# Kernel tuning notes

Measured on AMD Instinct MI355X. Metric: run time of the kernel, lower is better.

## Reference

```python
import jax, jax.numpy as jnp
import numpy as np

B, T, C, H = 2, 2048, 1024, 16
D = C // H  # head_dim = 64


def setup_inputs() -> dict:
    key = jax.random.key(0)
    ks = jax.random.split(key, 5)
    x = jax.random.normal(ks[0], (B, T, C), dtype=jnp.float32)
    # fused QKV projection: Linear(C, 3C)
    W_qkv = jax.random.normal(ks[1], (C, 3 * C), dtype=jnp.float32) / np.sqrt(C)
    b_qkv = jax.random.normal(ks[2], (3 * C,), dtype=jnp.float32) * 0.02
    # output projection: Linear(C, C)
    W_proj = jax.random.normal(ks[3], (C, C), dtype=jnp.float32) / np.sqrt(C)
    b_proj = jax.random.normal(ks[4], (C,), dtype=jnp.float32) * 0.02
    return {"x": x, "W_qkv": W_qkv, "b_qkv": b_qkv, "W_proj": W_proj, "b_proj": b_proj}


def reference(x, W_qkv, b_qkv, W_proj, b_proj):
    # fused QKV projection
    qkv = jnp.einsum("btc,cd->btd", x, W_qkv) + b_qkv  # [B,T,3C]
    q, k, v = jnp.split(qkv, 3, axis=-1)
    # [B,T,C] -> [B,H,T,D]
    def to_heads(t):
        return t.reshape(B, T, H, D).transpose(0, 2, 1, 3)
    q, k, v = to_heads(q), to_heads(k), to_heads(v)
    # causal scaled dot-product attention (SDPA default scale = 1/sqrt(head_dim))
    scale = 1.0 / np.sqrt(D).astype(np.float32)
    scores = jnp.einsum("bhqd,bhkd->bhqk", q, k) * scale  # [B,H,T,T]
    causal = jnp.tril(jnp.ones((T, T), dtype=bool))
    scores = jnp.where(causal, scores, jnp.finfo(scores.dtype).min)
    attn = jax.nn.softmax(scores, axis=-1)
    out = jnp.einsum("bhqk,bhkd->bhqd", attn, v)  # [B,H,T,D]
    out = out.transpose(0, 2, 1, 3).reshape(B, T, C)
    # output projection
    return jnp.einsum("btc,cd->btd", out, W_proj) + b_proj
```

## Files before the change

kernel.cpp:

```cpp
#include <hip/hip_runtime.h>
#include <hip/hip_bf16.h>

typedef __attribute__((ext_vector_type(8))) __bf16 bf16x8;
typedef __attribute__((ext_vector_type(8))) short short8;
typedef __attribute__((ext_vector_type(4))) float f32x4;
typedef __attribute__((ext_vector_type(16))) float f32x16;
typedef __attribute__((ext_vector_type(4))) short sh4;

typedef __attribute__((address_space(1))) void GVoid;
typedef __attribute__((address_space(3))) void LVoid;

#define NEGBIG (-1e30f)
#define SCL 0.18033688011112042f

constexpr int TT = 2048, CC = 1024, HH = 16, DD = 64, C3 = 3072;

__device__ __forceinline__ unsigned short f2bf(float f) {
  unsigned int i = __float_as_uint(f);
  return (unsigned short)((i + 0x7FFFu + ((i >> 16) & 1u)) >> 16);
}
__device__ __forceinline__ void async16(const void* g, void* l) {
  __builtin_amdgcn_global_load_lds((GVoid*)g, (LVoid*)l, 16, 0, 0);
}

__global__ __launch_bounds__(256) void cvt_bf16(
    const float* __restrict__ in, unsigned short* __restrict__ out, int n8)
{
  const int i = blockIdx.x * 256 + threadIdx.x;
  if (i >= n8) return;
  const float* p = in + (size_t)i * 8;
  f32x4 a = *(const f32x4*)p, b = *(const f32x4*)(p + 4);
  sh4 r0, r1;
  ((unsigned short*)&r0)[0] = f2bf(a[0]); ((unsigned short*)&r0)[1] = f2bf(a[1]);
  ((unsigned short*)&r0)[2] = f2bf(a[2]); ((unsigned short*)&r0)[3] = f2bf(a[3]);
  ((unsigned short*)&r1)[0] = f2bf(b[0]); ((unsigned short*)&r1)[1] = f2bf(b[1]);
  ((unsigned short*)&r1)[2] = f2bf(b[2]); ((unsigned short*)&r1)[3] = f2bf(b[3]);
  *(sh4*)(out + (size_t)i * 8) = r0;
  *(sh4*)(out + (size_t)i * 8 + 4) = r1;
}

__global__ __launch_bounds__(256) void transpose_cvt(
    const float* __restrict__ in, unsigned short* __restrict__ out, int R, int Cd)
{
  __shared__ __align__(16) unsigned short tile[64 * 72];
  const int r0 = blockIdx.y * 64, c0 = blockIdx.x * 64;
  const int tid = threadIdx.x;
#pragma unroll
  for (int r = 0; r < 2; ++r) {
    const int elem = r * 2048 + tid * 8;
    const int ii = elem >> 6, jj = elem & 63;
    const float* p = in + (size_t)(r0 + ii) * Cd + c0 + jj;
    f32x4 a = *(const f32x4*)p, b = *(const f32x4*)(p + 4);
    short8 v;
    ((unsigned short*)&v)[0] = f2bf(a[0]); ((unsigned short*)&v)[1] = f2bf(a[1]);
    ((unsigned short*)&v)[2] = f2bf(a[2]); ((unsigned short*)&v)[3] = f2bf(a[3]);
    ((unsigned short*)&v)[4] = f2bf(b[0]); ((unsigned short*)&v)[5] = f2bf(b[1]);
    ((unsigned short*)&v)[6] = f2bf(b[2]); ((unsigned short*)&v)[7] = f2bf(b[3]);
    *(short8*)&tile[ii * 72 + jj] = v;
  }
  __syncthreads();
#pragma unroll
  for (int r = 0; r < 2; ++r) {
    const int elem = r * 2048 + tid * 8;
    const int jj = elem >> 6, ii0 = elem & 63;
    short8 v;
#pragma unroll
    for (int e = 0; e < 8; ++e) ((unsigned short*)&v)[e] = tile[(ii0 + e) * 72 + jj];
    *(short8*)&out[(size_t)(c0 + jj) * R + r0 + ii0] = v;
  }
}

template <int MODE>
__global__ __launch_bounds__(256) void gemm_bt(
    const unsigned short* __restrict__ A,
    const unsigned short* __restrict__ Bt,
    const float* __restrict__ bias,
    void* __restrict__ Cp, unsigned short* __restrict__ Vt,
    int M, int N, int K, int lda)
{
  __shared__ __align__(16) unsigned short sA[2][128 * 32];
  __shared__ __align__(16) unsigned short sB[2][128 * 32];
  const int tid = threadIdx.x;
  const int w = tid >> 6, l = tid & 63, ln = l & 15, quad = l >> 4;
  const int wm = w >> 1, wn = w & 1;
  const int m0 = blockIdx.y * 128, n0 = blockIdx.x * 128;
  f32x4 acc[4][4] = {};

  const int elem0 = tid * 8;
  const int ar0 = elem0 >> 5, ac0 = elem0 & 31;
  const int ar1 = (2048 + elem0) >> 5, ac1 = ac0;

  async16(A  + (size_t)(m0 + ar0) * lda + ac0, &sA[0][w * 512]);
  async16(Bt + (size_t)(n0 + ar0) * K   + ac0, &sB[0][w * 512]);
  async16(A  + (size_t)(m0 + ar1) * lda + ac1, &sA[0][2048 + w * 512]);
  async16(Bt + (size_t)(n0 + ar1) * K   + ac1, &sB[0][2048 + w * 512]);
  __syncthreads();

  int buf = 0;
  for (int k0 = 0; k0 < K; k0 += 32, buf ^= 1) {
    if (k0 + 32 < K) {
      const int nb = buf ^ 1, kn = k0 + 32;
      async16(A  + (size_t)(m0 + ar0) * lda + kn + ac0, &sA[nb][w * 512]);
      async16(Bt + (size_t)(n0 + ar0) * K   + kn + ac0, &sB[nb][w * 512]);
      async16(A  + (size_t)(m0 + ar1) * lda + kn + ac1, &sA[nb][2048 + w * 512]);
      async16(Bt + (size_t)(n0 + ar1) * K   + kn + ac1, &sB[nb][2048 + w * 512]);
    }

    bf16x8 af[4], bfr[4];
#pragma unroll
    for (int i = 0; i < 4; i++)
      af[i] = *(const bf16x8*)&sA[buf][(wm * 64 + i * 16 + ln) * 32 + quad * 8];
#pragma unroll
    for (int j = 0; j < 4; j++)
      bfr[j] = *(const bf16x8*)&sB[buf][(wn * 64 + j * 16 + ln) * 32 + quad * 8];
#pragma unroll
    for (int i = 0; i < 4; i++)
#pragma unroll
      for (int j = 0; j < 4; j++)
        acc[i][j] = __builtin_amdgcn_mfma_f32_16x16x32_bf16(af[i], bfr[j], acc[i][j], 0, 0, 0);

    __syncthreads();
  }

  float bj[4];
#pragma unroll
  for (int j = 0; j < 4; j++) bj[j] = bias[n0 + wn * 64 + j * 16 + ln];

#pragma unroll
  for (int i = 0; i < 4; i++) {
#pragma unroll
    for (int j = 0; j < 4; j++) {
      const int gn = n0 + wn * 64 + j * 16 + ln;
      if (MODE == 0 && gn >= 2048) {
        const int hh = (gn >> 6) & 15, dd = gn & 63;
        const int gm0 = m0 + wm * 64 + i * 16 + quad * 4;
        const int bb = gm0 >> 11, t0 = gm0 & 2047;
        sh4 rv;
#pragma unroll
        for (int g = 0; g < 4; ++g)
          ((unsigned short*)&rv)[g] = f2bf(acc[i][j][g] + bj[j]);
        *(sh4*)&Vt[((size_t)((bb * HH + hh) * DD + dd)) * TT + t0] = rv;
      } else {
#pragma unroll
        for (int g = 0; g < 4; ++g) {
          const int gm = m0 + wm * 64 + i * 16 + quad * 4 + g;
          float v = acc[i][j][g] + bj[j];
          if (MODE == 0) {
            if (gn < 1024) v *= SCL;
            ((unsigned short*)Cp)[(size_t)gm * 2048 + gn] = f2bf(v);
          } else {
            ((float*)Cp)[(size_t)gm * N + gn] = v;
          }
        }
      }
    }
  }
}

__global__ __launch_bounds__(256) void gemm_n64(
    const unsigned short* __restrict__ A,
    const unsigned short* __restrict__ Bt,
    const float* __restrict__ bias,
    float* __restrict__ Cp, int M, int N, int K, int lda)
{
  __shared__ __align__(16) unsigned short sA[2][128 * 32];
  __shared__ __align__(16) unsigned short sB[2][64 * 32];
  const int tid = threadIdx.x;
  const int w = tid >> 6, l = tid & 63, ln = l & 15, quad = l >> 4;
  const int wm = w >> 1, wn = w & 1;
  const int m0 = blockIdx.y * 128, n0 = blockIdx.x * 64;
  f32x4 acc[4][2] = {};

  const int elem0 = tid * 8;
  const int ar0 = elem0 >> 5, ac0 = elem0 & 31;
  const int ar1 = (2048 + elem0) >> 5, ac1 = ac0;

  async16(A  + (size_t)(m0 + ar0) * lda + ac0, &sA[0][w * 512]);
  async16(A  + (size_t)(m0 + ar1) * lda + ac1, &sA[0][2048 + w * 512]);
  async16(Bt + (size_t)(n0 + ar0) * K   + ac0, &sB[0][w * 512]);
  __syncthreads();

  int buf = 0;
  for (int k0 = 0; k0 < K; k0 += 32, buf ^= 1) {
    if (k0 + 32 < K) {
      const int nb = buf ^ 1, kn = k0 + 32;
      async16(A  + (size_t)(m0 + ar0) * lda + kn + ac0, &sA[nb][w * 512]);
      async16(A  + (size_t)(m0 + ar1) * lda + kn + ac1, &sA[nb][2048 + w * 512]);
      async16(Bt + (size_t)(n0 + ar0) * K   + kn + ac0, &sB[nb][w * 512]);
    }

    bf16x8 af[4], bfr[2];
#pragma unroll
    for (int i = 0; i < 4; i++)
      af[i] = *(const bf16x8*)&sA[buf][(wm * 64 + i * 16 + ln) * 32 + quad * 8];
#pragma unroll
    for (int j = 0; j < 2; j++)
      bfr[j] = *(const bf16x8*)&sB[buf][(wn * 32 + j * 16 + ln) * 32 + quad * 8];
#pragma unroll
    for (int i = 0; i < 4; i++)
#pragma unroll
      for (int j = 0; j < 2; j++)
        acc[i][j] = __builtin_amdgcn_mfma_f32_16x16x32_bf16(af[i], bfr[j], acc[i][j], 0, 0, 0);

    __syncthreads();
  }

  float bj[2];
#pragma unroll
  for (int j = 0; j < 2; j++) bj[j] = bias[n0 + wn * 32 + j * 16 + ln];

#pragma unroll
  for (int i = 0; i < 4; i++)
#pragma unroll
    for (int g = 0; g < 4; ++g) {
      const int gm = m0 + wm * 64 + i * 16 + quad * 4 + g;
#pragma unroll
      for (int j = 0; j < 2; j++) {
        const int gn = n0 + wn * 32 + j * 16 + ln;
        Cp[(size_t)gm * N + gn] = acc[i][j][g] + bj[j];
      }
    }
}

__global__ __launch_bounds__(512) void attn2g(
    unsigned short* __restrict__ QK, const unsigned short* __restrict__ Vt)
{
  __shared__ __align__(16) unsigned short kt[2][2][64 * 72];
  __shared__ __align__(16) unsigned short vt[2][3][64 * 72];
  __shared__ float Ox[4][2][16][64];
  __shared__ float Lx[4][64];
  const int lid = blockIdx.y * gridDim.x + blockIdx.x;
  const int xcd = lid & 7, idx = lid >> 3;
  const int bh = xcd * 4 + (idx & 3);
  const int pair = idx >> 2;
  const int b = bh >> 4, h = bh & 15;
  const int tid = threadIdx.x;
  const int grp = tid >> 8, gtid = tid & 255;
  const int wg = (tid >> 6) & 3, l = tid & 63;
  const int c = l & 31, h2 = l >> 5;
  unsigned short*       Qp = QK + (size_t)b * TT * 2048 + h * DD;
  const unsigned short* Kp = QK + (size_t)b * TT * 2048 + CC + h * DD;
  const unsigned short* Vh = Vt + (size_t)bh * DD * TT;
  const int si0 = gtid >> 3, so = (gtid & 7) * 8;

  for (int ph = 0; ph < 2; ++ph) {
    const int qt = ph ? 15 - pair : pair;
    const int qbase = qt * 128 + wg * 32;
    const int qm = qbase + c - 4 * h2;
    bf16x8 qv[4];
#pragma unroll
    for (int ds = 0; ds < 4; ++ds)
      qv[ds] = *(const bf16x8*)&Qp[(size_t)(qbase + c) * 2048 + ds * 16 + h2 * 8];

    f32x16 oacc[2] = {};
    bf16x8 pA[4] = {};
    float lsum = 0.0f;
    const int nslot = qt + 1;
    int vm1 = 2, v0 = 0, vp1 = 1;

    __syncthreads();
#pragma unroll
    for (int r = 0; r < 2; ++r) {
      const int si = si0 + 32 * r;
      *(short8*)&kt[grp][0][si * 72 + so] =
          *(const short8*)&Kp[(size_t)(grp * 64 + si) * 2048 + so];
      *(short8*)&vt[grp][0][si * 72 + so] =
          *(const short8*)&Vh[(size_t)si * TT + grp * 64 + so];
    }
    __syncthreads();

    for (int slot = 0; slot < nslot; ++slot) {
      const int kb = 2 * slot + grp;
      const int ck = slot & 1;
      short8 pk[2], pv[2];
      if (slot + 1 < nslot) {
        const int kbn = kb + 2;
#pragma unroll
        for (int r = 0; r < 2; ++r) {
          const int si = si0 + 32 * r;
          pk[r] = *(const short8*)&Kp[(size_t)(kbn * 64 + si) * 2048 + so];
          pv[r] = *(const short8*)&Vh[(size_t)si * TT + kbn * 64 + so];
        }
      }
      const bool qk_act = (kb * 64 <= qbase + 31);
      f32x16 sacc[2];
      if (qk_act) {
        __builtin_amdgcn_s_setprio(1);
#pragma unroll
        for (int kg = 0; kg < 2; ++kg) {
          f32x16 sa = {};
#pragma unroll
          for (int ds = 0; ds < 4; ++ds) {
            bf16x8 kf = *(const bf16x8*)&kt[grp][ck][(kg * 32 + c) * 72 + ds * 16 + h2 * 8];
            sa = __builtin_amdgcn_mfma_f32_32x32x16_bf16(kf, qv[ds], sa, 0, 0, 0);
          }
          sacc[kg] = sa;
        }
        __builtin_amdgcn_s_setprio(0);
      }
      if (slot > 0 && (kb - 2) * 64 <= qbase + 31) {
        const unsigned short* vp = vt[grp][vm1];
        __builtin_amdgcn_s_setprio(1);
#pragma unroll
        for (int dg = 0; dg < 2; ++dg)
#pragma unroll
          for (int ks = 0; ks < 4; ++ks) {
            bf16x8 vf = *(const bf16x8*)&vp[(dg * 32 + c) * 72 + ks * 16 + h2 * 8];
            oacc[dg] = __builtin_amdgcn_mfma_f32_32x32x16_bf16(pA[ks], vf, oacc[dg], 0, 0, 0);
          }
        __builtin_amdgcn_s_setprio(0);
      }
      if (qk_act) {
        const bool need_mask = (kb * 64 + 63 > qbase);
        float pe[2][16];
#pragma unroll
        for (int kg = 0; kg < 2; ++kg)
#pragma unroll
          for (int rr = 0; rr < 16; ++rr) {
            float sv = sacc[kg][rr];
            if (need_mask) {
              const int krel = kb * 64 + kg * 32 + (rr & 3) + 8 * (rr >> 2);
              if (krel > qm) sv = NEGBIG;
            }
            float e;
            asm("v_exp_f32 %0, %1" : "=v"(e) : "v"(sv));
            pe[kg][rr] = e;
            lsum += e;
          }
        unsigned W0[2][4], W1[2][4];
#pragma unroll
        for (int kg = 0; kg < 2; ++kg)
#pragma unroll
          for (int r4 = 0; r4 < 4; ++r4) {
            asm("v_cvt_pk_bf16_f32 %0, %1, %2"
                : "=v"(W0[kg][r4]) : "v"(pe[kg][4 * r4 + 0]), "v"(pe[kg][4 * r4 + 1]));
            asm("v_cvt_pk_bf16_f32 %0, %1, %2"
                : "=v"(W1[kg][r4]) : "v"(pe[kg][4 * r4 + 2]), "v"(pe[kg][4 * r4 + 3]));
          }
#pragma unroll
        for (int ks = 0; ks < 4; ++ks) {
          const int kg = ks >> 1, sel = ks & 1;
          unsigned a0 = W0[kg][2 * sel], b0 = W0[kg][2 * sel + 1];
          unsigned a1 = W1[kg][2 * sel], b1 = W1[kg][2 * sel + 1];
          asm("v_permlane32_swap_b32 %0, %1" : "+v"(a0), "+v"(b0));
          asm("v_permlane32_swap_b32 %0, %1" : "+v"(a1), "+v"(b1));
          unsigned wds[4] = {a0, a1, b0, b1};
          pA[ks] = *(const bf16x8*)wds;
        }
      }
      if (slot + 1 < nslot) {
#pragma unroll
        for (int r = 0; r < 2; ++r) {
          const int si = si0 + 32 * r;
          *(short8*)&kt[grp][1 - ck][si * 72 + so] = pk[r];
          *(short8*)&vt[grp][vp1][si * 72 + so] = pv[r];
        }
      }
      __syncthreads();
      const int t_ = vm1; vm1 = v0; v0 = vp1; vp1 = t_;
    }
    const int kb_last = 2 * qt + grp;
    if (kb_last * 64 <= qbase + 31) {
      const unsigned short* vp = vt[grp][vm1];
#pragma unroll
      for (int dg = 0; dg < 2; ++dg)
#pragma unroll
        for (int ks = 0; ks < 4; ++ks) {
          bf16x8 vf = *(const bf16x8*)&vp[(dg * 32 + c) * 72 + ks * 16 + h2 * 8];
          oacc[dg] = __builtin_amdgcn_mfma_f32_32x32x16_bf16(pA[ks], vf, oacc[dg], 0, 0, 0);
        }
    }
    lsum += __shfl_xor(lsum, 32);
    if (grp == 1) {
#pragma unroll
      for (int dg = 0; dg < 2; ++dg)
#pragma unroll
        for (int rr = 0; rr < 16; ++rr) Ox[wg][dg][rr][l] = oacc[dg][rr];
      Lx[wg][l] = lsum;
    }
    __syncthreads();
    if (grp == 0) {
      const float inv = 1.0f / (lsum + Lx[wg][l]);
#pragma unroll
      for (int dg = 0; dg < 2; ++dg)
#pragma unroll
        for (int rr = 0; rr < 16; ++rr) oacc[dg][rr] += Ox[wg][dg][rr][l];
#pragma unroll
      for (int rr = 0; rr < 16; ++rr) {
        const int q_rel = (rr & 3) + 8 * (rr >> 2) + 4 * h2;
        const float iq = __shfl(inv, q_rel);
        const size_t trow = qbase + q_rel;
#pragma unroll
        for (int dg = 0; dg < 2; ++dg)
          Qp[trow * 2048 + dg * 32 + c] = f2bf(oacc[dg][rr] * iq);
      }
    }
  }
}

extern "C" void kernel_launch(void* const* d_in, const int* in_sizes, int n_in,
                              void* d_out, int out_size, void* d_ws, size_t ws_size,
                              hipStream_t stream)
{
  (void)in_sizes; (void)n_in; (void)out_size; (void)ws_size;
  const float* x     = (const float*)d_in[0];
  const float* Wqkv  = (const float*)d_in[1];
  const float* bqkv  = (const float*)d_in[2];
  const float* Wproj = (const float*)d_in[3];
  const float* bproj = (const float*)d_in[4];

  unsigned short* QK     = (unsigned short*)d_ws;
  unsigned short* WqkvT  = QK + (size_t)4096 * 2048;
  unsigned short* WprojT = WqkvT;
  unsigned short* Vt = (unsigned short*)d_out;
  unsigned short* xb = Vt + (size_t)32 * 64 * 2048;

  cvt_bf16<<<dim3(4096 * 1024 / 8 / 256), 256, 0, stream>>>(x, xb, 4096 * 1024 / 8);
  transpose_cvt<<<dim3(C3 / 64, CC / 64), 256, 0, stream>>>(Wqkv, WqkvT, CC, C3);
  gemm_bt<0><<<dim3(C3 / 128, 4096 / 128), 256, 0, stream>>>(
      xb, WqkvT, bqkv, QK, Vt, 4096, C3, CC, CC);
  transpose_cvt<<<dim3(CC / 64, CC / 64), 256, 0, stream>>>(Wproj, WprojT, CC, CC);
  attn2g<<<dim3(8, 2 * HH), 512, 0, stream>>>(QK, Vt);
  gemm_n64<<<dim3(CC / 64, 4096 / 128), 256, 0, stream>>>(
      QK, WprojT, bproj, (float*)d_out, 4096, CC, CC, 2048);
}
```

Before: 180.5 us.

## Process two KV tiles per barrier with a 4-deep LDS ring buffer

Restructures the attention inner loop so each iteration handles two key/value tiles between barriers, using a four-slot shared-memory ring for K and V per group, which halves the number of __syncthreads calls. The old software pipeline, which overlapped the PV MFMA of the previous tile with the QK of the current one, is replaced by a straight per-tile compute lambda that does QK, softmax and PV in sequence. The LDS arrays are merged into one union buffer that is reused for the final cross-group reduction, so total LDS grows (144 KB). Risks are lower occupancy and the loss of the cross-tile MFMA/VALU overlap.

```diff
diff --git a/kernel.cpp b/kernel.cpp
--- a/kernel.cpp
+++ b/kernel.cpp
@@ -225,10 +225,9 @@
 __global__ __launch_bounds__(512) void attn2g(
     unsigned short* __restrict__ QK, const unsigned short* __restrict__ Vt)
 {
-  __shared__ __align__(16) unsigned short kt[2][2][64 * 72];
-  __shared__ __align__(16) unsigned short vt[2][3][64 * 72];
-  __shared__ float Ox[4][2][16][64];
-  __shared__ float Lx[4][64];
+  __shared__ __align__(16) unsigned short smem[73728];
+  float* Ms  = (float*)smem;
+  float* Lxp = (float*)smem + 8192;
   const int lid = blockIdx.y * gridDim.x + blockIdx.x;
   const int xcd = lid & 7, idx = lid >> 3;
   const int bh = xcd * 4 + (idx & 3);
@@ -242,6 +241,8 @@
   const unsigned short* Kp = QK + (size_t)b * TT * 2048 + CC + h * DD;
   const unsigned short* Vh = Vt + (size_t)bh * DD * TT;
   const int si0 = gtid >> 3, so = (gtid & 7) * 8;
+  unsigned short* kt0 = smem + grp * 4 * 4608;
+  unsigned short* vt0 = smem + 36864 + grp * 4 * 4608;
 
   for (int ph = 0; ph < 2; ++ph) {
     const int qt = ph ? 15 - pair : pair;
@@ -253,138 +254,158 @@
       qv[ds] = *(const bf16x8*)&Qp[(size_t)(qbase + c) * 2048 + ds * 16 + h2 * 8];
 
     f32x16 oacc[2] = {};
-    bf16x8 pA[4] = {};
     float lsum = 0.0f;
-    const int nslot = qt + 1;
-    int vm1 = 2, v0 = 0, vp1 = 1;
+    const int ntile = qt + 1;
+
+    auto compute = [&](int t) {
+      const int kb = 2 * t + grp;
+      if (kb * 64 > qbase + 31) return;
+      const unsigned short* ktp = kt0 + (t & 3) * 4608;
+      const unsigned short* vtp = vt0 + (t & 3) * 4608;
+      f32x16 sacc[2];
+      __builtin_amdgcn_s_setprio(1);
+#pragma unroll
+      for (int kg = 0; kg < 2; ++kg) {
+        f32x16 sa = {};
+#pragma unroll
+        for (int ds = 0; ds < 4; ++ds) {
+          bf16x8 kf = *(const bf16x8*)&ktp[(kg * 32 + c) * 72 + ds * 16 + h2 * 8];
+          sa = __builtin_amdgcn_mfma_f32_32x32x16_bf16(kf, qv[ds], sa, 0, 0, 0);
+        }
+        sacc[kg] = sa;
+      }
+      __builtin_amdgcn_s_setprio(0);
+      const bool need_mask = (kb * 64 + 63 > qbase);
+      float pe[2][16];
+#pragma unroll
+      for (int kg = 0; kg < 2; ++kg)
+#pragma unroll
+        for (int rr = 0; rr < 16; ++rr) {
+          float sv = sacc[kg][rr];
+          if (need_mask) {
+            const int krel = kb * 64 + kg * 32 + (rr & 3) + 8 * (rr >> 2);
+            if (krel > qm) sv = NEGBIG;
+          }
+          float e;
+          asm("v_exp_f32 %0, %1" : "=v"(e) : "v"(sv));
+          pe[kg][rr] = e;
+          lsum += e;
+        }
+      unsigned W0[2][4], W1[2][4];
+#pragma unroll
+      for (int kg = 0; kg < 2; ++kg)
+#pragma unroll
+        for (int r4 = 0; r4 < 4; ++r4) {
+          asm("v_cvt_pk_bf16_f32 %0, %1, %2"
+              : "=v"(W0[kg][r4]) : "v"(pe[kg][4 * r4 + 0]), "v"(pe[kg][4 * r4 + 1]));
+          asm("v_cvt_pk_bf16_f32 %0, %1, %2"
+              : "=v"(W1[kg][r4]) : "v"(pe[kg][4 * r4 + 2]), "v"(pe[kg][4 * r4 + 3]));
+        }
+      bf16x8 pA[4];
+#pragma unroll
+      for (int ks = 0; ks < 4; ++ks) {
+        const int kg = ks >> 1, sel = ks & 1;
+        unsigned a0 = W0[kg][2 * sel], b0 = W0[kg][2 * sel + 1];
+        unsigned a1 = W1[kg][2 * sel], b1 = W1[kg][2 * sel + 1];
+        asm("v_permlane32_swap_b32 %0, %1" : "+v"(a0), "+v"(b0));
+        asm("v_permlane32_swap_b32 %0, %1" : "+v"(a1), "+v"(b1));
+        unsigned wds[4] = {a0, a1, b0, b1};
+        pA[ks] = *(const bf16x8*)wds;
+      }
+      __builtin_amdgcn_s_setprio(1);
+#pragma unroll
+      for (int dg = 0; dg < 2; ++dg)
+#pragma unroll
+        for (int ks = 0; ks < 4; ++ks) {
+          bf16x8 vf = *(const bf16x8*)&vtp[(dg * 32 + c) * 72 + ks * 16 + h2 * 8];
+          oacc[dg] = __builtin_amdgcn_mfma_f32_32x32x16_bf16(pA[ks], vf, oacc[dg], 0, 0, 0);
+        }
+      __builtin_amdgcn_s_setprio(0);
+    };
 
     __syncthreads();
-#pragma unroll
-    for (int r = 0; r < 2; ++r) {
-      const int si = si0 + 32 * r;
-      *(short8*)&kt[grp][0][si * 72 + so] =
-          *(const short8*)&Kp[(size_t)(grp * 64 + si) * 2048 + so];
-      *(short8*)&vt[grp][0][si * 72 + so] =
-          *(const short8*)&Vh[(size_t)si * TT + grp * 64 + so];
-    }
-    __syncthreads();
-
-    for (int slot = 0; slot < nslot; ++slot) {
-      const int kb = 2 * slot + grp;
-      const int ck = slot & 1;
-      short8 pk[2], pv[2];
-      if (slot + 1 < nslot) {
-        const int kbn = kb + 2;
+    {
+      const int kb0 = grp;
+#pragma unroll
+      for (int r = 0; r < 2; ++r) {
+        const int si = si0 + 32 * r;
+        *(short8*)&kt0[si * 72 + so] = *(const short8*)&Kp[(size_t)(kb0 * 64 + si) * 2048 + so];
+        *(short8*)&vt0[si * 72 + so] = *(const short8*)&Vh[(size_t)si * TT + kb0 * 64 + so];
+      }
+      if (ntile > 1) {
+        const int kb1 = 2 + grp;
 #pragma unroll
         for (int r = 0; r < 2; ++r) {
           const int si = si0 + 32 * r;
-          pk[r] = *(const short8*)&Kp[(size_t)(kbn * 64 + si) * 2048 + so];
-          pv[r] = *(const short8*)&Vh[(size_t)si * TT + kbn * 64 + so];
-        }
-      }
-      const bool qk_act = (kb * 64 <= qbase + 31);
-      f32x16 sacc[2];
-      if (qk_act) {
-        __builtin_amdgcn_s_setprio(1);
-#pragma unroll
-        for (int kg = 0; kg < 2; ++kg) {
-          f32x16 sa = {};
-#pragma unroll
-          for (int ds = 0; ds < 4; ++ds) {
-            bf16x8 kf = *(const bf16x8*)&kt[grp][ck][(kg * 32 + c) * 72 + ds * 16 + h2 * 8];
-            sa = __builtin_amdgcn_mfma_f32_32x32x16_bf16(kf, qv[ds], sa, 0, 0, 0);
-          }
-          sacc[kg] = sa;
-        }
-        __builtin_amdgcn_s_setprio(0);
-      }
-      if (slot > 0 && (kb - 2) * 64 <= qbase + 31) {
-        const unsigned short* vp = vt[grp][vm1];
-        __builtin_amdgcn_s_setprio(1);
-#pragma unroll
-        for (int dg = 0; dg < 2; ++dg)
-#pragma unroll
-          for (int ks = 0; ks < 4; ++ks) {
-            bf16x8 vf = *(const bf16x8*)&vp[(dg * 32 + c) * 72 + ks * 16 + h2 * 8];
-            oacc[dg] = __builtin_amdgcn_mfma_f32_32x32x16_bf16(pA[ks], vf, oacc[dg], 0, 0, 0);
-          }
-        __builtin_amdgcn_s_setprio(0);
-      }
-      if (qk_act) {
-        const bool need_mask = (kb * 64 + 63 > qbase);
-        float pe[2][16];
-#pragma unroll
-        for (int kg = 0; kg < 2; ++kg)
-#pragma unroll
-          for (int rr = 0; rr < 16; ++rr) {
-            float sv = sacc[kg][rr];
-            if (need_mask) {
-              const int krel = kb * 64 + kg * 32 + (rr & 3) + 8 * (rr >> 2);
-              if (krel > qm) sv = NEGBIG;
-            }
-            float e;
-            asm("v_exp_f32 %0, %1" : "=v"(e) : "v"(sv));
-            pe[kg][rr] = e;
-            lsum += e;
-          }
-        unsigned W0[2][4], W1[2][4];
-#pragma unroll
-        for (int kg = 0; kg < 2; ++kg)
-#pragma unroll
-          for (int r4 = 0; r4 < 4; ++r4) {
-            asm("v_cvt_pk_bf16_f32 %0, %1, %2"
-                : "=v"(W0[kg][r4]) : "v"(pe[kg][4 * r4 + 0]), "v"(pe[kg][4 * r4 + 1]));
-            asm("v_cvt_pk_bf16_f32 %0, %1, %2"
-                : "=v"(W1[kg][r4]) : "v"(pe[kg][4 * r4 + 2]), "v"(pe[kg][4 * r4 + 3]));
-          }
-#pragma unroll
-        for (int ks = 0; ks < 4; ++ks) {
-          const int kg = ks >> 1, sel = ks & 1;
-          unsigned a0 = W0[kg][2 * sel], b0 = W0[kg][2 * sel + 1];
-          unsigned a1 = W1[kg][2 * sel], b1 = W1[kg][2 * sel + 1];
-          asm("v_permlane32_swap_b32 %0, %1" : "+v"(a0), "+v"(b0));
-          asm("v_permlane32_swap_b32 %0, %1" : "+v"(a1), "+v"(b1));
-          unsigned wds[4] = {a0, a1, b0, b1};
-          pA[ks] = *(const bf16x8*)wds;
-        }
-      }
-      if (slot + 1 < nslot) {
+          *(short8*)&kt0[4608 + si * 72 + so] =
+              *(const short8*)&Kp[(size_t)(kb1 * 64 + si) * 2048 + so];
+          *(short8*)&vt0[4608 + si * 72 + so] =
+              *(const short8*)&Vh[(size_t)si * TT + kb1 * 64 + so];
+        }
+      }
+    }
+    __syncthreads();
+
+    const int S = (ntile + 1) >> 1;
+    for (int s = 0; s < S; ++s) {
+      const int t2 = 2 * s + 2, t3 = 2 * s + 3;
+      short8 pk[2], pv[2];
+      if (t2 < ntile) {
+        const int kb = 2 * t2 + grp;
 #pragma unroll
         for (int r = 0; r < 2; ++r) {
           const int si = si0 + 32 * r;
-          *(short8*)&kt[grp][1 - ck][si * 72 + so] = pk[r];
-          *(short8*)&vt[grp][vp1][si * 72 + so] = pv[r];
+          pk[r] = *(const short8*)&Kp[(size_t)(kb * 64 + si) * 2048 + so];
+          pv[r] = *(const short8*)&Vh[(size_t)si * TT + kb * 64 + so];
+        }
+      }
+      compute(2 * s);
+      if (t2 < ntile) {
+#pragma unroll
+        for (int r = 0; r < 2; ++r) {
+          const int si = si0 + 32 * r;
+          *(short8*)&kt0[(t2 & 3) * 4608 + si * 72 + so] = pk[r];
+          *(short8*)&vt0[(t2 & 3) * 4608 + si * 72 + so] = pv[r];
+        }
+      }
+      if (t3 < ntile) {
+        const int kb = 2 * t3 + grp;
+#pragma unroll
+        for (int r = 0; r < 2; ++r) {
+          const int si = si0 + 32 * r;
+          pk[r] = *(const short8*)&Kp[(size_t)(kb * 64 + si) * 2048 + so];
+          pv[r] = *(const short8*)&Vh[(size_t)si * TT + kb * 64 + so];
+        }
+      }
+      if (2 * s + 1 < ntile) compute(2 * s + 1);
+      if (t3 < ntile) {
+#pragma unroll
+        for (int r = 0; r < 2; ++r) {
+          const int si = si0 + 32 * r;
+          *(short8*)&kt0[(t3 & 3) * 4608 + si * 72 + so] = pk[r];
+          *(short8*)&vt0[(t3 & 3) * 4608 + si * 72 + so] = pv[r];
         }
       }
       __syncthreads();
-      const int t_ = vm1; vm1 = v0; v0 = vp1; vp1 = t_;
-    }
-    const int kb_last = 2 * qt + grp;
-    if (kb_last * 64 <= qbase + 31) {
-      const unsigned short* vp = vt[grp][vm1];
-#pragma unroll
-      for (int dg = 0; dg < 2; ++dg)
-#pragma unroll
-        for (int ks = 0; ks < 4; ++ks) {
-          bf16x8 vf = *(const bf16x8*)&vp[(dg * 32 + c) * 72 + ks * 16 + h2 * 8];
-          oacc[dg] = __builtin_amdgcn_mfma_f32_32x32x16_bf16(pA[ks], vf, oacc[dg], 0, 0, 0);
-        }
-    }
+    }
+
     lsum += __shfl_xor(lsum, 32);
     if (grp == 1) {
 #pragma unroll
       for (int dg = 0; dg < 2; ++dg)
 #pragma unroll
-        for (int rr = 0; rr < 16; ++rr) Ox[wg][dg][rr][l] = oacc[dg][rr];
-      Lx[wg][l] = lsum;
+        for (int rr = 0; rr < 16; ++rr)
+          Ms[((wg * 2 + dg) * 16 + rr) * 64 + l] = oacc[dg][rr];
+      Lxp[wg * 64 + l] = lsum;
     }
     __syncthreads();
     if (grp == 0) {
-      const float inv = 1.0f / (lsum + Lx[wg][l]);
+      const float inv = 1.0f / (lsum + Lxp[wg * 64 + l]);
 #pragma unroll
       for (int dg = 0; dg < 2; ++dg)
 #pragma unroll
-        for (int rr = 0; rr < 16; ++rr) oacc[dg][rr] += Ox[wg][dg][rr][l];
+        for (int rr = 0; rr < 16; ++rr)
+          oacc[dg][rr] += Ms[((wg * 2 + dg) * 16 + rr) * 64 + l];
 #pragma unroll
       for (int rr = 0; rr < 16; ++rr) {
         const int q_rel = (rr & 3) + 8 * (rr >> 2) + 4 * h2;
```

Measured after the change: 177.3 us. About the same (-1.8%).
